# Kernel tuning notes

Hardware: AMD Instinct MI355X
Metric: run time of the kernel (lower is better)

Reference implementation:

```python
import jax, jax.numpy as jnp
import numpy as np

VOLRADIUS = 64.0
DT = 1.0 / VOLRADIUS          # normalized step size (dt / volradius)
NSTEPS = 64                   # covers t in [0, 1.0) at step DT


def setup_inputs() -> dict:
    key = jax.random.key(0)
    ks = jax.random.split(key, 8)
    B, H, W, K, M = 1, 128, 128, 32, 16
    # ray origins near volume center, unit directions
    raypos = 0.2 * jax.random.normal(ks[0], (B, H, W, 3), jnp.float32)
    rd = jax.random.normal(ks[1], (B, H, W, 3), jnp.float32)
    raydir = rd / jnp.linalg.norm(rd, axis=-1, keepdims=True)
    tmin = jnp.zeros((B, H, W), jnp.float32)
    tmax = 0.9 + 0.1 * jax.random.uniform(ks[2], (B, H, W), dtype=jnp.float32)
    tminmax = jnp.stack([tmin, tmax], axis=-1)
    # primitive poses: positions, rotations (orthonormal via QR), inverse-scales
    primpos = 0.3 * jax.random.normal(ks[3], (B, K, 3), jnp.float32)
    A = jax.random.normal(ks[4], (B, K, 3, 3), jnp.float32)
    primrot, _ = jnp.linalg.qr(A)
    primscale = 1.0 + 2.0 * jax.random.uniform(ks[5], (B, K, 3), dtype=jnp.float32)
    # RGBA voxel payload per primitive; alpha channel nonnegative (decoder emits nonneg density)
    template = jax.random.normal(ks[6], (B, K, 4, M, M, M), jnp.float32)
    template = template.at[:, :, 3].set(2.0 * jax.nn.softplus(template[:, :, 3]))
    return dict(raypos=raypos, raydir=raydir, tminmax=tminmax, primpos=primpos,
                primrot=primrot, primscale=primscale, template=template)


def _trilinear(template, y):
    # template [B,K,C,M,M,M]; y [B,R,K,3] normalized coords in [-1,1] (align_corners)
    B, K, C, M = template.shape[0], template.shape[1], template.shape[2], template.shape[3]
    g = (y + 1.0) * 0.5 * (M - 1)
    i0 = jnp.clip(jnp.floor(g), 0, M - 2).astype(jnp.int32)
    f = jnp.clip(g - i0.astype(g.dtype), 0.0, 1.0)
    i1 = i0 + 1
    bidx = jnp.arange(B)[:, None, None]
    kidx = jnp.arange(K)[None, None, :]

    def corner(iz, iy, ix):
        # advanced-index gather -> [B,R,K,C]
        return template[bidx, kidx, :, iz, iy, ix]

    fz, fy, fx = f[..., 0:1], f[..., 1:2], f[..., 2:3]
    i0z, i0y, i0x = i0[..., 0], i0[..., 1], i0[..., 2]
    i1z, i1y, i1x = i1[..., 0], i1[..., 1], i1[..., 2]
    v = ((1 - fz) * (1 - fy) * (1 - fx) * corner(i0z, i0y, i0x)
         + (1 - fz) * (1 - fy) * fx * corner(i0z, i0y, i1x)
         + (1 - fz) * fy * (1 - fx) * corner(i0z, i1y, i0x)
         + (1 - fz) * fy * fx * corner(i0z, i1y, i1x)
         + fz * (1 - fy) * (1 - fx) * corner(i1z, i0y, i0x)
         + fz * (1 - fy) * fx * corner(i1z, i0y, i1x)
         + fz * fy * (1 - fx) * corner(i1z, i1y, i0x)
         + fz * fy * fx * corner(i1z, i1y, i1x))
    return v  # [B,R,K,C]


def reference(raypos, raydir, tminmax, primpos, primrot, primscale, template):
    B, H, W, _ = raypos.shape
    R = H * W
    rp = raypos.reshape(B, R, 3)
    rd = raydir.reshape(B, R, 3)
    tmm = tminmax.reshape(B, R, 2)
    tmin, tmax = tmm[..., 0:1], tmm[..., 1:2]

    def step(carry, i):
        rgb, alpha = carry
        t = tmin + i * DT                                   # [B,R,1]
        pos = rp + rd * t                                   # [B,R,3]
        xl = pos[:, :, None, :] - primpos[:, None, :, :]    # [B,R,K,3]
        yloc = jnp.einsum('bkij,brkj->brki', primrot, xl) * primscale[:, None, :, :]
        inside = jnp.all(jnp.abs(yloc) <= 1.0, axis=-1, keepdims=True).astype(rgb.dtype)
        samp = (_trilinear(template, yloc) * inside).sum(axis=2)   # [B,R,4]
        srgb, salpha = samp[..., :3], samp[..., 3:4]
        valid = (t < tmax).astype(rgb.dtype)
        # clamped additive compositing (Neural Volumes / MVP)
        newalpha = jnp.clip(alpha + salpha * DT * valid, 0.0, 1.0)
        contrib = newalpha - alpha
        return (rgb + srgb * contrib, newalpha), None

    init = (jnp.zeros((B, R, 3), raypos.dtype), jnp.zeros((B, R, 1), raypos.dtype))
    (rgb, alpha), _ = jax.lax.scan(step, init, jnp.arange(NSTEPS, dtype=raypos.dtype))

    rayrgba = jnp.concatenate([rgb, alpha], axis=-1).reshape(B, H, W, 4)
    rayrgba = jnp.transpose(rayrgba, (0, 3, 1, 2))   # [B,4,H,W]
    rayrgb = rayrgba[:, :3]
    rayalpha = rayrgba[:, 3:4]
    return rayrgb, rayalpha, rayrgba
```

## Files before the change

kernel.cpp:

```cpp
#include <hip/hip_runtime.h>
#include <hip/hip_fp16.h>


namespace {

constexpr float kDT  = 1.0f / 64.0f;
constexpr int   kVox = 32 * 4096;

struct H4 { __half2 lo, hi; };
struct __attribute__((aligned(8))) H4x2 { __half2 l0, h0, l1, h1; };

__global__ __launch_bounds__(256) void transpose_tmpl_h(
    const float* __restrict__ tmpl, H4* __restrict__ wsH)
{
    const int idx = blockIdx.x * 256 + threadIdx.x;
    const int k   = idx >> 12;
    const int rem = idx & 4095;
    const float* src = tmpl + k * 16384 + rem;
    H4 v;
    v.lo = __floats2half2_rn(src[0],    src[4096]);
    v.hi = __floats2half2_rn(src[8192], src[12288]);
    wsH[idx] = v;
}

__device__ __forceinline__ __half2 lerp2(__half2 a, __half2 b, __half2 f) {
    return __hfma2(f, __hsub2(b, a), a);
}

__global__ __launch_bounds__(256) void raymarch9(
    const float* __restrict__ raypos,
    const float* __restrict__ raydir,
    const float* __restrict__ tminmax,
    const float* __restrict__ primpos,
    const float* __restrict__ primrot,
    const float* __restrict__ primscale,
    const H4* __restrict__ wsH,
    float* __restrict__ out,
    int R)
{
    const int lane   = threadIdx.x & 63;
    const int wid    = threadIdx.x >> 6;
    const int k      = lane & 31;
    const int parity = lane >> 5;
    const int ray    = blockIdx.x * 4 + wid;

    const float rpx = raypos[ray * 3 + 0];
    const float rpy = raypos[ray * 3 + 1];
    const float rpz = raypos[ray * 3 + 2];
    const float rdx = raydir[ray * 3 + 0];
    const float rdy = raydir[ray * 3 + 1];
    const float rdz = raydir[ray * 3 + 2];
    const float tmin = tminmax[ray * 2 + 0];
    const float tmax = tminmax[ray * 2 + 1];

    float A0, A1, A2, D0, D1, D2;
    {
        const float ox = rpx - primpos[k * 3 + 0];
        const float oy = rpy - primpos[k * 3 + 1];
        const float oz = rpz - primpos[k * 3 + 2];
        const float s0 = primscale[k * 3 + 0];
        const float s1 = primscale[k * 3 + 1];
        const float s2 = primscale[k * 3 + 2];
        const float* rk = primrot + k * 9;
        A0 = (rk[0] * ox + rk[1] * oy + rk[2] * oz) * s0;
        D0 = (rk[0] * rdx + rk[1] * rdy + rk[2] * rdz) * s0;
        A1 = (rk[3] * ox + rk[4] * oy + rk[5] * oz) * s1;
        D1 = (rk[3] * rdx + rk[4] * rdy + rk[5] * rdz) * s1;
        A2 = (rk[6] * ox + rk[7] * oy + rk[8] * oz) * s2;
        D2 = (rk[6] * rdx + rk[7] * rdy + rk[8] * rdz) * s2;
    }

    const H4* __restrict__ tbase = wsH + k * 4096;

    float alpha = 0.f;
    float r0 = 0.f, r1 = 0.f, r2 = 0.f;

    for (int j = 0; j < 32; ++j) {
        const float t0 = fmaf((float)(2 * j), kDT, tmin);
        if (t0 >= tmax || alpha >= 1.0f) break;

        const float tl = fmaf((float)(2 * j + parity), kDT, tmin);
        const float y0 = fmaf(D0, tl, A0);
        const float y1 = fmaf(D1, tl, A1);
        const float y2 = fmaf(D2, tl, A2);
        const bool inside = (tl < tmax) && fabsf(y0) <= 1.0f
                         && fabsf(y1) <= 1.0f && fabsf(y2) <= 1.0f;
        if (__ballot(inside) == 0ull) continue;

        float s0 = 0.f, s1 = 0.f, s2 = 0.f, s3 = 0.f;
        if (inside) {
            const float gz = fmaf(y0, 7.5f, 7.5f);
            const float gy = fmaf(y1, 7.5f, 7.5f);
            const float gx = fmaf(y2, 7.5f, 7.5f);
            const int iz = min((int)gz, 14);
            const int iy = min((int)gy, 14);
            const int ix = min((int)gx, 14);
            const float fz = fminf(gz - (float)iz, 1.0f);
            const float fy = fminf(gy - (float)iy, 1.0f);
            const float fx = fminf(gx - (float)ix, 1.0f);

            const H4* tp = tbase + (iz * 256 + iy * 16 + ix);
            const H4x2 p00 = *(const H4x2*)(tp + 0);
            const H4x2 p01 = *(const H4x2*)(tp + 16);
            const H4x2 p10 = *(const H4x2*)(tp + 256);
            const H4x2 p11 = *(const H4x2*)(tp + 272);

            const __half2 hz = __float2half2_rn(fz);
            const __half2 hy = __float2half2_rn(fy);
            const __half2 hx = __float2half2_rn(fx);

            const __half2 q0l0 = lerp2(p00.l0, p10.l0, hz);
            const __half2 q0h0 = lerp2(p00.h0, p10.h0, hz);
            const __half2 q0l1 = lerp2(p00.l1, p10.l1, hz);
            const __half2 q0h1 = lerp2(p00.h1, p10.h1, hz);
            const __half2 q1l0 = lerp2(p01.l0, p11.l0, hz);
            const __half2 q1h0 = lerp2(p01.h0, p11.h0, hz);
            const __half2 q1l1 = lerp2(p01.l1, p11.l1, hz);
            const __half2 q1h1 = lerp2(p01.h1, p11.h1, hz);

            const __half2 ul0 = lerp2(q0l0, q1l0, hy);
            const __half2 uh0 = lerp2(q0h0, q1h0, hy);
            const __half2 ul1 = lerp2(q0l1, q1l1, hy);
            const __half2 uh1 = lerp2(q0h1, q1h1, hy);

            const __half2 vl = lerp2(ul0, ul1, hx);
            const __half2 vh = lerp2(uh0, uh1, hx);

            const float2 fLo = __half22float2(vl);
            const float2 fHi = __half22float2(vh);
            s0 = fLo.x; s1 = fLo.y; s2 = fHi.x; s3 = fHi.y;
        }

        float tot = s3;
        #pragma unroll
        for (int m = 1; m < 32; m <<= 1) tot += __shfl_xor(tot, m);
        const float other = __shfl_xor(tot, 32);
        const float te = parity ? other : tot;
        const float to = parity ? tot : other;

        const float t1v = fmaf((float)(2 * j + 1), kDT, tmin);
        const float a_e = te * kDT;
        const float a_o = (t1v < tmax) ? to * kDT : 0.0f;
        const float na1 = fminf(alpha + a_e, 1.0f);
        const float c_e = na1 - alpha;
        const float na2 = fminf(na1 + a_o, 1.0f);
        const float c_o = na2 - na1;
        alpha = na2;

        const float contrib = parity ? c_o : c_e;
        r0 = fmaf(s0, contrib, r0);
        r1 = fmaf(s1, contrib, r1);
        r2 = fmaf(s2, contrib, r2);
    }

    #pragma unroll
    for (int m = 1; m < 64; m <<= 1) {
        r0 += __shfl_xor(r0, m);
        r1 += __shfl_xor(r1, m);
        r2 += __shfl_xor(r2, m);
    }

    if (lane == 0) {
        out[0 * R + ray] = r0;
        out[1 * R + ray] = r1;
        out[2 * R + ray] = r2;
        out[3 * R + ray] = alpha;
        out[4 * R + ray] = r0;
        out[5 * R + ray] = r1;
        out[6 * R + ray] = r2;
        out[7 * R + ray] = alpha;
    }
}

__global__ __launch_bounds__(256) void raymarch_fb(
    const float* __restrict__ raypos, const float* __restrict__ raydir,
    const float* __restrict__ tminmax, const float* __restrict__ primpos,
    const float* __restrict__ primrot, const float* __restrict__ primscale,
    const float* __restrict__ tmpl, float* __restrict__ out, int R)
{
    const int lane = threadIdx.x & 63;
    const int wid  = threadIdx.x >> 6;
    const int k    = lane & 31;
    const int half = lane >> 5;
    const int ray  = blockIdx.x * 8 + wid * 2 + half;

    const float rpx = raypos[ray*3+0], rpy = raypos[ray*3+1], rpz = raypos[ray*3+2];
    const float rdx = raydir[ray*3+0], rdy = raydir[ray*3+1], rdz = raydir[ray*3+2];
    const float tmin = tminmax[ray*2+0], tmax = tminmax[ray*2+1];

    float A0,A1,A2,D0,D1,D2;
    {
        const float ox = rpx - primpos[k*3+0], oy = rpy - primpos[k*3+1], oz = rpz - primpos[k*3+2];
        const float s0 = primscale[k*3+0], s1 = primscale[k*3+1], s2 = primscale[k*3+2];
        const float* rk = primrot + k*9;
        A0 = (rk[0]*ox+rk[1]*oy+rk[2]*oz)*s0; D0 = (rk[0]*rdx+rk[1]*rdy+rk[2]*rdz)*s0;
        A1 = (rk[3]*ox+rk[4]*oy+rk[5]*oz)*s1; D1 = (rk[3]*rdx+rk[4]*rdy+rk[5]*rdz)*s1;
        A2 = (rk[6]*ox+rk[7]*oy+rk[8]*oz)*s2; D2 = (rk[6]*rdx+rk[7]*rdy+rk[8]*rdz)*s2;
    }
    float alpha = 0.f, r0 = 0.f, r1 = 0.f, r2 = 0.f;
    for (int i = 0; i < 64; ++i) {
        const float t = fmaf((float)i, kDT, tmin);
        const bool live = (t < tmax) && (alpha < 1.0f);
        if (__ballot(live) == 0ull) break;
        const float y0 = fmaf(D0,t,A0), y1 = fmaf(D1,t,A1), y2 = fmaf(D2,t,A2);
        const bool inside = live && fabsf(y0)<=1.f && fabsf(y1)<=1.f && fabsf(y2)<=1.f;
        if (__ballot(inside) == 0ull) continue;
        float s0=0.f,s1=0.f,s2=0.f,s3=0.f;
        if (inside) {
            const float gz=(y0+1.f)*7.5f, gy=(y1+1.f)*7.5f, gx=(y2+1.f)*7.5f;
            const int iz=(int)fminf(floorf(gz),14.f), iy=(int)fminf(floorf(gy),14.f), ix=(int)fminf(floorf(gx),14.f);
            const float fz=fminf(gz-(float)iz,1.f), fy=fminf(gy-(float)iy,1.f), fx=fminf(gx-(float)ix,1.f);
            const float oz_=1.f-fz, oy_=1.f-fy, ox_=1.f-fx;
            const float w000=oz_*oy_*ox_, w001=oz_*oy_*fx, w010=oz_*fy*ox_, w011=oz_*fy*fx;
            const float w100=fz*oy_*ox_, w101=fz*oy_*fx, w110=fz*fy*ox_, w111=fz*fy*fx;
            const float* tp = tmpl + k*16384 + iz*256 + iy*16 + ix;
            float acc[4];
            #pragma unroll
            for (int c = 0; c < 4; ++c) {
                const float* tc = tp + c*4096;
                acc[c] = w000*tc[0]+w001*tc[1]+w010*tc[16]+w011*tc[17]
                       + w100*tc[256]+w101*tc[257]+w110*tc[272]+w111*tc[273];
            }
            s0=acc[0]; s1=acc[1]; s2=acc[2]; s3=acc[3];
        }
        float tot3 = s3;
        #pragma unroll
        for (int m = 1; m < 32; m <<= 1) tot3 += __shfl_xor(tot3, m);
        const float na = fminf(fmaf(tot3, kDT, alpha), 1.0f);
        const float contrib = na - alpha;
        alpha = na;
        r0 = fmaf(s0, contrib, r0); r1 = fmaf(s1, contrib, r1); r2 = fmaf(s2, contrib, r2);
    }
    #pragma unroll
    for (int m = 1; m < 32; m <<= 1) {
        r0 += __shfl_xor(r0, m); r1 += __shfl_xor(r1, m); r2 += __shfl_xor(r2, m);
    }
    if (k == 0) {
        out[0*R+ray]=r0; out[1*R+ray]=r1; out[2*R+ray]=r2; out[3*R+ray]=alpha;
        out[4*R+ray]=r0; out[5*R+ray]=r1; out[6*R+ray]=r2; out[7*R+ray]=alpha;
    }
}

}

extern "C" void kernel_launch(void* const* d_in, const int* in_sizes, int n_in,
                              void* d_out, int out_size, void* d_ws, size_t ws_size,
                              hipStream_t stream) {
    const float* raypos    = (const float*)d_in[0];
    const float* raydir    = (const float*)d_in[1];
    const float* tminmax   = (const float*)d_in[2];
    const float* primpos   = (const float*)d_in[3];
    const float* primrot   = (const float*)d_in[4];
    const float* primscale = (const float*)d_in[5];
    const float* tmpl      = (const float*)d_in[6];
    float* out = (float*)d_out;

    const int R = in_sizes[0] / 3;
    const size_t needH = (size_t)kVox * sizeof(H4);

    if (ws_size >= needH) {
        H4* wsH = (H4*)d_ws;
        transpose_tmpl_h<<<dim3(kVox / 256), dim3(256), 0, stream>>>(tmpl, wsH);
        raymarch9<<<dim3(R / 4), dim3(256), 0, stream>>>(
            raypos, raydir, tminmax, primpos, primrot, primscale, wsH, out, R);
    } else {
        raymarch_fb<<<dim3(R / 8), dim3(256), 0, stream>>>(
            raypos, raydir, tminmax, primpos, primrot, primscale, tmpl, out, R);
    }
}
```

Baseline: 88.47 us.

## Map lanes to ray steps, cull primitives by slab test, scan alpha

```diff
diff --git a/kernel.cpp b/kernel.cpp
--- a/kernel.cpp
+++ b/kernel.cpp
@@ -27,7 +27,11 @@
     return __hfma2(f, __hsub2(b, a), a);
 }
 
-__global__ __launch_bounds__(256) void raymarch9(
+__device__ __forceinline__ float bcast_lane(float v, int srcLane) {
+    return __uint_as_float(__builtin_amdgcn_readlane(__float_as_uint(v), srcLane));
+}
+
+__global__ __launch_bounds__(256) void raymarch11(
     const float* __restrict__ raypos,
     const float* __restrict__ raydir,
     const float* __restrict__ tminmax,
@@ -38,11 +42,10 @@
     float* __restrict__ out,
     int R)
 {
-    const int lane   = threadIdx.x & 63;
-    const int wid    = threadIdx.x >> 6;
-    const int k      = lane & 31;
-    const int parity = lane >> 5;
-    const int ray    = blockIdx.x * 4 + wid;
+    const int lane = threadIdx.x & 63;
+    const int wid  = threadIdx.x >> 6;
+    const int ray  = blockIdx.x * 4 + wid;
+    const int k    = lane & 31;
 
     const float rpx = raypos[ray * 3 + 0];
     const float rpy = raypos[ray * 3 + 1];
@@ -70,24 +73,41 @@
         D2 = (rk[6] * rdx + rk[7] * rdy + rk[8] * rdz) * s2;
     }
 
-    const H4* __restrict__ tbase = wsH + k * 4096;
-
-    float alpha = 0.f;
-    float r0 = 0.f, r1 = 0.f, r2 = 0.f;
-
-    for (int j = 0; j < 32; ++j) {
-        const float t0 = fmaf((float)(2 * j), kDT, tmin);
-        if (t0 >= tmax || alpha >= 1.0f) break;
-
-        const float tl = fmaf((float)(2 * j + parity), kDT, tmin);
-        const float y0 = fmaf(D0, tl, A0);
-        const float y1 = fmaf(D1, tl, A1);
-        const float y2 = fmaf(D2, tl, A2);
-        const bool inside = (tl < tmax) && fabsf(y0) <= 1.0f
-                         && fabsf(y1) <= 1.0f && fabsf(y2) <= 1.0f;
-        if (__ballot(inside) == 0ull) continue;
-
-        float s0 = 0.f, s1 = 0.f, s2 = 0.f, s3 = 0.f;
+    unsigned mask;
+    {
+        const float i0 = 1.0f / D0, i1 = 1.0f / D1, i2 = 1.0f / D2;
+        const float a0 = (-1.0f - A0) * i0, b0 = (1.0f - A0) * i0;
+        const float a1 = (-1.0f - A1) * i1, b1 = (1.0f - A1) * i1;
+        const float a2 = (-1.0f - A2) * i2, b2 = (1.0f - A2) * i2;
+        const float tEnd = fminf(tmax, fmaf(63.0f, kDT, tmin));
+        const float lo = fmaxf(fmaxf(fminf(a0, b0), fminf(a1, b1)),
+                               fmaxf(fminf(a2, b2), tmin));
+        const float hi = fminf(fminf(fmaxf(a0, b0), fmaxf(a1, b1)),
+                               fminf(fmaxf(a2, b2), tEnd));
+        const bool active = lo <= hi + 2.0f * kDT;
+        mask = (unsigned)(__ballot(active) & 0xffffffffull);
+    }
+
+    const float t_l = fmaf((float)lane, kDT, tmin);
+
+    float s0 = 0.f, s1 = 0.f, s2 = 0.f, s3 = 0.f;
+
+    while (mask) {
+        const int kk = __builtin_ctz(mask);
+        mask &= mask - 1;
+
+        const float bA0 = bcast_lane(A0, kk);
+        const float bA1 = bcast_lane(A1, kk);
+        const float bA2 = bcast_lane(A2, kk);
+        const float bD0 = bcast_lane(D0, kk);
+        const float bD1 = bcast_lane(D1, kk);
+        const float bD2 = bcast_lane(D2, kk);
+
+        const float y0 = fmaf(bD0, t_l, bA0);
+        const float y1 = fmaf(bD1, t_l, bA1);
+        const float y2 = fmaf(bD2, t_l, bA2);
+        const bool inside = fabsf(y0) <= 1.0f && fabsf(y1) <= 1.0f
+                         && fabsf(y2) <= 1.0f;
         if (inside) {
             const float gz = fmaf(y0, 7.5f, 7.5f);
             const float gy = fmaf(y1, 7.5f, 7.5f);
@@ -99,7 +119,7 @@
             const float fy = fminf(gy - (float)iy, 1.0f);
             const float fx = fminf(gx - (float)ix, 1.0f);
 
-            const H4* tp = tbase + (iz * 256 + iy * 16 + ix);
+            const H4* tp = wsH + (kk << 12) + (iz * 256 + iy * 16 + ix);
             const H4x2 p00 = *(const H4x2*)(tp + 0);
             const H4x2 p01 = *(const H4x2*)(tp + 16);
             const H4x2 p10 = *(const H4x2*)(tp + 256);
@@ -128,37 +148,32 @@
 
             const float2 fLo = __half22float2(vl);
             const float2 fHi = __half22float2(vh);
-            s0 = fLo.x; s1 = fLo.y; s2 = fHi.x; s3 = fHi.y;
+            s0 += fLo.x; s1 += fLo.y; s2 += fHi.x; s3 += fHi.y;
         }
-
-        float tot = s3;
-        #pragma unroll
-        for (int m = 1; m < 32; m <<= 1) tot += __shfl_xor(tot, m);
-        const float other = __shfl_xor(tot, 32);
-        const float te = parity ? other : tot;
-        const float to = parity ? tot : other;
-
-        const float t1v = fmaf((float)(2 * j + 1), kDT, tmin);
-        const float a_e = te * kDT;
-        const float a_o = (t1v < tmax) ? to * kDT : 0.0f;
-        const float na1 = fminf(alpha + a_e, 1.0f);
-        const float c_e = na1 - alpha;
-        const float na2 = fminf(na1 + a_o, 1.0f);
-        const float c_o = na2 - na1;
-        alpha = na2;
-
-        const float contrib = parity ? c_o : c_e;
-        r0 = fmaf(s0, contrib, r0);
-        r1 = fmaf(s1, contrib, r1);
-        r2 = fmaf(s2, contrib, r2);
-    }
-
+    }
+
+    const bool valid = t_l < tmax;
+    const float inc = valid ? s3 * kDT : 0.0f;
+    float p = inc;
+    #pragma unroll
+    for (int d = 1; d < 64; d <<= 1) {
+        const float n = __shfl_up(p, d, 64);
+        if (lane >= d) p += n;
+    }
+    float ex = __shfl_up(p, 1, 64);
+    if (lane == 0) ex = 0.0f;
+    const float contrib = fminf(p, 1.0f) - fminf(ex, 1.0f);
+
+    float r0 = s0 * contrib;
+    float r1 = s1 * contrib;
+    float r2 = s2 * contrib;
     #pragma unroll
     for (int m = 1; m < 64; m <<= 1) {
         r0 += __shfl_xor(r0, m);
         r1 += __shfl_xor(r1, m);
         r2 += __shfl_xor(r2, m);
     }
+    const float alpha = fminf(__shfl(p, 63, 64), 1.0f);
 
     if (lane == 0) {
         out[0 * R + ray] = r0;
@@ -261,7 +276,7 @@
     if (ws_size >= needH) {
         H4* wsH = (H4*)d_ws;
         transpose_tmpl_h<<<dim3(kVox / 256), dim3(256), 0, stream>>>(tmpl, wsH);
-        raymarch9<<<dim3(R / 4), dim3(256), 0, stream>>>(
+        raymarch11<<<dim3(R / 4), dim3(256), 0, stream>>>(
             raypos, raydir, tminmax, primpos, primrot, primscale, wsH, out, R);
     } else {
         raymarch_fb<<<dim3(R / 8), dim3(256), 0, stream>>>(
```

Result: slower. 133.8 us (+51.2%).

## Software-pipeline texel gathers one step ahead and use DPP reductions

Applied to the files above, without the earlier changes.

```diff
diff --git a/kernel.cpp b/kernel.cpp
--- a/kernel.cpp
+++ b/kernel.cpp
@@ -27,7 +27,22 @@
     return __hfma2(f, __hsub2(b, a), a);
 }
 
-__global__ __launch_bounds__(256) void raymarch9(
+template<int CTRL>
+__device__ __forceinline__ float dpp_add(float v) {
+    return v + __int_as_float(__builtin_amdgcn_update_dpp(
+        0, __float_as_int(v), CTRL, 0xF, 0xF, true));
+}
+
+__device__ __forceinline__ float half_sum32(float v) {
+    v = dpp_add<0xB1>(v);
+    v = dpp_add<0x4E>(v);
+    v = dpp_add<0x141>(v);
+    v = dpp_add<0x140>(v);
+    v += __int_as_float(__builtin_amdgcn_ds_swizzle(__float_as_int(v), 0x401F));
+    return v;
+}
+
+__global__ __launch_bounds__(256) void raymarch12(
     const float* __restrict__ raypos,
     const float* __restrict__ raydir,
     const float* __restrict__ tminmax,
@@ -75,90 +90,112 @@
     float alpha = 0.f;
     float r0 = 0.f, r1 = 0.f, r2 = 0.f;
 
-    for (int j = 0; j < 32; ++j) {
-        const float t0 = fmaf((float)(2 * j), kDT, tmin);
-        if (t0 >= tmax || alpha >= 1.0f) break;
-
-        const float tl = fmaf((float)(2 * j + parity), kDT, tmin);
-        const float y0 = fmaf(D0, tl, A0);
-        const float y1 = fmaf(D1, tl, A1);
-        const float y2 = fmaf(D2, tl, A2);
-        const bool inside = (tl < tmax) && fabsf(y0) <= 1.0f
-                         && fabsf(y1) <= 1.0f && fabsf(y2) <= 1.0f;
-        if (__ballot(inside) == 0ull) continue;
-
-        float s0 = 0.f, s1 = 0.f, s2 = 0.f, s3 = 0.f;
-        if (inside) {
-            const float gz = fmaf(y0, 7.5f, 7.5f);
-            const float gy = fmaf(y1, 7.5f, 7.5f);
-            const float gx = fmaf(y2, 7.5f, 7.5f);
-            const int iz = min((int)gz, 14);
-            const int iy = min((int)gy, 14);
-            const int ix = min((int)gx, 14);
-            const float fz = fminf(gz - (float)iz, 1.0f);
-            const float fy = fminf(gy - (float)iy, 1.0f);
-            const float fx = fminf(gx - (float)ix, 1.0f);
-
-            const H4* tp = tbase + (iz * 256 + iy * 16 + ix);
-            const H4x2 p00 = *(const H4x2*)(tp + 0);
-            const H4x2 p01 = *(const H4x2*)(tp + 16);
-            const H4x2 p10 = *(const H4x2*)(tp + 256);
-            const H4x2 p11 = *(const H4x2*)(tp + 272);
-
-            const __half2 hz = __float2half2_rn(fz);
-            const __half2 hy = __float2half2_rn(fy);
-            const __half2 hx = __float2half2_rn(fx);
-
-            const __half2 q0l0 = lerp2(p00.l0, p10.l0, hz);
-            const __half2 q0h0 = lerp2(p00.h0, p10.h0, hz);
-            const __half2 q0l1 = lerp2(p00.l1, p10.l1, hz);
-            const __half2 q0h1 = lerp2(p00.h1, p10.h1, hz);
-            const __half2 q1l0 = lerp2(p01.l0, p11.l0, hz);
-            const __half2 q1h0 = lerp2(p01.h0, p11.h0, hz);
-            const __half2 q1l1 = lerp2(p01.l1, p11.l1, hz);
-            const __half2 q1h1 = lerp2(p01.h1, p11.h1, hz);
-
-            const __half2 ul0 = lerp2(q0l0, q1l0, hy);
-            const __half2 uh0 = lerp2(q0h0, q1h0, hy);
-            const __half2 ul1 = lerp2(q0l1, q1l1, hy);
-            const __half2 uh1 = lerp2(q0h1, q1h1, hy);
-
-            const __half2 vl = lerp2(ul0, ul1, hx);
-            const __half2 vh = lerp2(uh0, uh1, hx);
-
-            const float2 fLo = __half22float2(vl);
-            const float2 fHi = __half22float2(vh);
-            s0 = fLo.x; s1 = fLo.y; s2 = fHi.x; s3 = fHi.y;
+    bool  inA, inB;
+    int   adA, adB;
+    float fzA, fyA, fxA, fzB, fyB, fxB;
+    H4x2  a00, a01, a10, a11, b00, b01, b10, b11;
+
+#define COORDS(J, IN, AD, FZ, FY, FX)                                    \
+    {                                                                    \
+        const float tl = fmaf((float)(2 * (J) + parity), kDT, tmin);     \
+        const float y0 = fmaf(D0, tl, A0);                               \
+        const float y1 = fmaf(D1, tl, A1);                               \
+        const float y2 = fmaf(D2, tl, A2);                               \
+        IN = ((J) < 32) && (tl < tmax) && fabsf(y0) <= 1.0f              \
+           && fabsf(y1) <= 1.0f && fabsf(y2) <= 1.0f;                    \
+        const float gz = fmaf(y0, 7.5f, 7.5f);                           \
+        const float gy = fmaf(y1, 7.5f, 7.5f);                           \
+        const float gx = fmaf(y2, 7.5f, 7.5f);                           \
+        const int iz = min((int)gz, 14);                                 \
+        const int iy = min((int)gy, 14);                                 \
+        const int ix = min((int)gx, 14);                                 \
+        FZ = fminf(gz - (float)iz, 1.0f);                                \
+        FY = fminf(gy - (float)iy, 1.0f);                                \
+        FX = fminf(gx - (float)ix, 1.0f);                                \
+        AD = iz * 256 + iy * 16 + ix;                                    \
+    }
+
+#define PREF(IN, AD, P00, P01, P10, P11)                                 \
+    if (IN) {                                                            \
+        const H4* tp = tbase + (AD);                                     \
+        P00 = *(const H4x2*)(tp + 0);                                    \
+        P01 = *(const H4x2*)(tp + 16);                                   \
+        P10 = *(const H4x2*)(tp + 256);                                  \
+        P11 = *(const H4x2*)(tp + 272);                                  \
+    }
+
+#define CONSUME(J, IN, FZ, FY, FX, P00, P01, P10, P11)                   \
+    {                                                                    \
+        float s0 = 0.f, s1 = 0.f, s2 = 0.f, s3 = 0.f;                    \
+        if (IN) {                                                        \
+            const __half2 hz = __float2half2_rn(FZ);                     \
+            const __half2 hy = __float2half2_rn(FY);                     \
+            const __half2 hx = __float2half2_rn(FX);                     \
+            const __half2 q0l0 = lerp2(P00.l0, P10.l0, hz);              \
+            const __half2 q0h0 = lerp2(P00.h0, P10.h0, hz);              \
+            const __half2 q0l1 = lerp2(P00.l1, P10.l1, hz);              \
+            const __half2 q0h1 = lerp2(P00.h1, P10.h1, hz);              \
+            const __half2 q1l0 = lerp2(P01.l0, P11.l0, hz);              \
+            const __half2 q1h0 = lerp2(P01.h0, P11.h0, hz);              \
+            const __half2 q1l1 = lerp2(P01.l1, P11.l1, hz);              \
+            const __half2 q1h1 = lerp2(P01.h1, P11.h1, hz);              \
+            const __half2 ul0 = lerp2(q0l0, q1l0, hy);                   \
+            const __half2 uh0 = lerp2(q0h0, q1h0, hy);                   \
+            const __half2 ul1 = lerp2(q0l1, q1l1, hy);                   \
+            const __half2 uh1 = lerp2(q0h1, q1h1, hy);                   \
+            const __half2 vl = lerp2(ul0, ul1, hx);                      \
+            const __half2 vh = lerp2(uh0, uh1, hx);                      \
+            const float2 fLo = __half22float2(vl);                       \
+            const float2 fHi = __half22float2(vh);                       \
+            s0 = fLo.x; s1 = fLo.y; s2 = fHi.x; s3 = fHi.y;              \
+        }                                                                \
+        if (__ballot(IN)) {                                              \
+            float tot = half_sum32(s3);                                  \
+            const float other = __shfl_xor(tot, 32);                     \
+            const float te = parity ? other : tot;       \
+            const float to = parity ? tot : other;       \
+              \
+            const float na1 = fminf(fmaf(te, kDT, alpha), 1.0f);         \
+            const float c_e = na1 - alpha;                               \
+            const float na2 = fminf(fmaf(to, kDT, na1), 1.0f);           \
+            const float c_o = na2 - na1;                                 \
+            alpha = na2;                                                 \
+            const float contrib = parity ? c_o : c_e;                    \
+            r0 = fmaf(s0, contrib, r0);                                  \
+            r1 = fmaf(s1, contrib, r1);                                  \
+            r2 = fmaf(s2, contrib, r2);                                  \
+        }                                                                \
+    }
+
+    COORDS(0, inA, adA, fzA, fyA, fxA);
+    PREF(inA, adA, a00, a01, a10, a11);
+
+    for (int j = 0; ; ) {
+        COORDS(j + 1, inB, adB, fzB, fyB, fxB);
+        PREF(inB, adB, b00, b01, b10, b11);
+        CONSUME(j, inA, fzA, fyA, fxA, a00, a01, a10, a11);
+        ++j;
+        {
+            const float t0 = fmaf((float)(2 * j), kDT, tmin);
+            if (j >= 32 || t0 >= tmax || alpha >= 1.0f) break;
         }
-
-        float tot = s3;
-        #pragma unroll
-        for (int m = 1; m < 32; m <<= 1) tot += __shfl_xor(tot, m);
-        const float other = __shfl_xor(tot, 32);
-        const float te = parity ? other : tot;
-        const float to = parity ? tot : other;
-
-        const float t1v = fmaf((float)(2 * j + 1), kDT, tmin);
-        const float a_e = te * kDT;
-        const float a_o = (t1v < tmax) ? to * kDT : 0.0f;
-        const float na1 = fminf(alpha + a_e, 1.0f);
-        const float c_e = na1 - alpha;
-        const float na2 = fminf(na1 + a_o, 1.0f);
-        const float c_o = na2 - na1;
-        alpha = na2;
-
-        const float contrib = parity ? c_o : c_e;
-        r0 = fmaf(s0, contrib, r0);
-        r1 = fmaf(s1, contrib, r1);
-        r2 = fmaf(s2, contrib, r2);
-    }
-
-    #pragma unroll
-    for (int m = 1; m < 64; m <<= 1) {
-        r0 += __shfl_xor(r0, m);
-        r1 += __shfl_xor(r1, m);
-        r2 += __shfl_xor(r2, m);
-    }
+        COORDS(j + 1, inA, adA, fzA, fyA, fxA);
+        PREF(inA, adA, a00, a01, a10, a11);
+        CONSUME(j, inB, fzB, fyB, fxB, b00, b01, b10, b11);
+        ++j;
+        {
+            const float t0 = fmaf((float)(2 * j), kDT, tmin);
+            if (j >= 32 || t0 >= tmax || alpha >= 1.0f) break;
+        }
+    }
+
+#undef COORDS
+#undef PREF
+#undef CONSUME
+
+    r0 = half_sum32(r0); r0 += __shfl_xor(r0, 32);
+    r1 = half_sum32(r1); r1 += __shfl_xor(r1, 32);
+    r2 = half_sum32(r2); r2 += __shfl_xor(r2, 32);
 
     if (lane == 0) {
         out[0 * R + ray] = r0;
@@ -261,7 +298,7 @@
     if (ws_size >= needH) {
         H4* wsH = (H4*)d_ws;
         transpose_tmpl_h<<<dim3(kVox / 256), dim3(256), 0, stream>>>(tmpl, wsH);
-        raymarch9<<<dim3(R / 4), dim3(256), 0, stream>>>(
+        raymarch12<<<dim3(R / 4), dim3(256), 0, stream>>>(
             raypos, raydir, tminmax, primpos, primrot, primscale, wsH, out, R);
     } else {
         raymarch_fb<<<dim3(R / 8), dim3(256), 0, stream>>>(
```

Result: slower. 90.35 us (+2.1%).
